# Kernel tuning notes

Hardware: AMD Instinct MI355X
Metric: run time of the kernel (lower is better)

## Reference

```python
import jax, jax.numpy as jnp
import numpy as np

HID = 256
N_HEADS = 4
ATTN_DIM = HID // N_HEADS  # 64
B, S = 64, 512
NEG = -1e10


def setup_inputs() -> dict:
    key = jax.random.key(0)
    ks = jax.random.split(key, 12)
    def lin(k, fan_in, shape):
        bound = 1.0 / np.sqrt(fan_in)
        return jax.random.uniform(k, shape, jnp.float32, -bound, bound)
    return {
        "query": jax.random.normal(ks[0], (B, S, HID), jnp.float32),
        "key": jax.random.normal(ks[1], (B, S, HID), jnp.float32),
        "value": jax.random.normal(ks[2], (B, S, HID), jnp.float32),
        "mask": jax.random.randint(ks[3], (B, 1, S, S), 0, 2, jnp.int32),
        "Wq": lin(ks[4], HID, (HID, HID)), "bq": lin(ks[5], HID, (HID,)),
        "Wk": lin(ks[6], HID, (HID, HID)), "bk": lin(ks[7], HID, (HID,)),
        "Wv": lin(ks[8], HID, (HID, ATTN_DIM)), "bv": lin(ks[9], HID, (ATTN_DIM,)),
        "Wh": lin(ks[10], ATTN_DIM, (ATTN_DIM, HID)), "bh": lin(ks[11], ATTN_DIM, (HID,)),
    }


def reference(query, key, value, mask, Wq, bq, Wk, bk, Wv, bv, Wh, bh):
    b = query.shape[0]
    scale = jnp.sqrt(jnp.asarray(ATTN_DIM, query.dtype))
    Q = (query @ Wq + bq).reshape(b, -1, N_HEADS, ATTN_DIM).transpose(0, 2, 1, 3)  # [B,H,Sq,d]
    K = (key @ Wk + bk).reshape(b, -1, N_HEADS, ATTN_DIM).transpose(0, 2, 1, 3)    # [B,H,Sk,d]
    V = value @ Wv + bv                                                            # [B,Sk,d]
    energy = jnp.einsum('bhqd,bhkd->bhqk', Q, K) / scale
    energy = jnp.where(mask == 0, jnp.asarray(NEG, energy.dtype), energy)
    probs = jax.nn.softmax(energy, axis=-1)          # [B,H,Sq,Sk]
    attention = jnp.mean(probs, axis=1)              # head-mean, [B,Sq,Sk]
    # dropout is identity in eval mode
    output = jnp.einsum('bqk,bkd->bqd', attention, V) @ Wh + bh  # [B,Sq,HID]
    return output, attention
```

## Files before the change

### kernel.cpp

```cpp
#include <hip/hip_runtime.h>

#define NB 64
#define SS 512
#define HIDD 256
#define NHEADS 4
#define ADIM 64
#define NTOT 576

typedef __attribute__((ext_vector_type(8))) short short8v;
typedef __attribute__((ext_vector_type(4))) float f32x4;

#define MFMA16(A, B, C) __builtin_amdgcn_mfma_f32_16x16x32_bf16(A, B, C, 0, 0, 0)
#define AS1 __attribute__((address_space(1)))
#define AS3 __attribute__((address_space(3)))

__device__ __forceinline__ void g2l16(void* lds, const void* g) {
    __builtin_amdgcn_global_load_lds((const AS1 unsigned*)g,
                                     (AS3 unsigned*)lds, 16, 0, 0);
}

__device__ __forceinline__ void bsplit(float x, short& hi, short& lo) {
    unsigned u = __float_as_uint(x);
    unsigned uh = (u + 0x8000u) & 0xFFFF0000u;
    hi = (short)(uh >> 16);
    float r = x - __uint_as_float(uh);
    lo = (short)((__float_as_uint(r) + 0x8000u) >> 16);
}

__device__ __forceinline__ void bsplit_v(float x, short8v& vh, short8v& vl, int i) {
    short h, l;
    bsplit(x, h, l);
    vh[i] = h;
    vl[i] = l;
}

__device__ __forceinline__ short bf16r(float x) {
    return (short)((__float_as_uint(x) + 0x8000u) >> 16);
}

__device__ __forceinline__ int frag_addr(int bb, int hh, int s, int d) {
    const int t16 = s >> 4, rk = s & 15;
    const int ks2 = d >> 5, lgk = (d >> 3) & 3, e8 = d & 7;
    return ((((bb * 4 + hh) * 32 + t16) * 2 + ks2) * 64 + rk + 16 * lgk) * 8 + e8;
}

__global__ __launch_bounds__(256) void prep_weights(
    const float* __restrict__ Wq, const float* __restrict__ Wk,
    const float* __restrict__ Wv, const float* __restrict__ Wh,
    short* __restrict__ WT_hi, short* __restrict__ WT_lo,
    short* __restrict__ WhT)
{
    const int bx = blockIdx.x;
    if (bx < NTOT) {
        const int idx = bx * 256 + threadIdx.x;
        const int n = idx >> 8, k = idx & 255;
        float v;
        if (n < 256)      v = Wq[k * 256 + n];
        else if (n < 512) v = Wk[k * 256 + (n - 256)];
        else              v = Wv[k * 64 + (n - 512)];
        short h, l;
        bsplit(v, h, l);
        WT_hi[idx] = h;
        WT_lo[idx] = l;
    } else {
        const int idx2 = (bx - NTOT) * 256 + threadIdx.x;
        const int n = idx2 >> 6, d = idx2 & 63;
        WhT[idx2] = bf16r(Wh[d * HIDD + n]);
    }
}

__global__ __launch_bounds__(256) void qkv_qk(
    const float* __restrict__ query, const float* __restrict__ key,
    const short* __restrict__ WT_hi, const short* __restrict__ WT_lo,
    const float* __restrict__ bq, const float* __restrict__ bk,
    short* __restrict__ Qhi, short* __restrict__ Khi)
{
    __shared__ short Ws_h[2][128 * 32];
    __shared__ short Ws_l[2][128 * 32];

    const int bm = blockIdx.x * 64;
    const int y = blockIdx.y;
    const int t = y >> 1;
    const int half = y & 1;
    const int nrow0 = t * 256 + half * 128;
    const float* A = t ? key : query;
    const float* biasp = t ? bk : bq;
    short* Dhi = t ? Khi : Qhi;

    const int tid = threadIdx.x;
    const int w = tid >> 6, l = tid & 63;
    const int l15 = l & 15, lg = l >> 4;
    const int wbase = tid & 192;

    auto stageWT = [&](int buf, int kc) {
#pragma unroll
        for (int i = 0; i < 2; ++i) {
            const int g = i * 256 + tid;
            const int row = g >> 2;
            const int p = g & 3;
            const int sl = p ^ (row & 3);
            const size_t goff = (size_t)(nrow0 + row) * HIDD + kc * 32 + sl * 8;
            g2l16(&Ws_h[buf][(i * 256 + wbase) * 8], WT_hi + goff);
            g2l16(&Ws_l[buf][(i * 256 + wbase) * 8], WT_lo + goff);
        }
    };

    const float* arow = A + (size_t)(bm + w * 16 + l15) * HIDD + lg * 8;

    f32x4 acc[8];
#pragma unroll
    for (int jn = 0; jn < 8; ++jn) acc[jn] = (f32x4){0.f, 0.f, 0.f, 0.f};

    float4 a0c = *reinterpret_cast<const float4*>(arow);
    float4 a1c = *reinterpret_cast<const float4*>(arow + 4);
    stageWT(0, 0);
    __syncthreads();

    int cur = 0;
#pragma unroll
    for (int kc = 0; kc < 8; ++kc) {
        float4 a0n, a1n;
        if (kc < 7) {
            a0n = *reinterpret_cast<const float4*>(arow + (kc + 1) * 32);
            a1n = *reinterpret_cast<const float4*>(arow + (kc + 1) * 32 + 4);
            stageWT(cur ^ 1, kc + 1);
        }

        short8v ah, al;
        bsplit_v(a0c.x, ah, al, 0);
        bsplit_v(a0c.y, ah, al, 1);
        bsplit_v(a0c.z, ah, al, 2);
        bsplit_v(a0c.w, ah, al, 3);
        bsplit_v(a1c.x, ah, al, 4);
        bsplit_v(a1c.y, ah, al, 5);
        bsplit_v(a1c.z, ah, al, 6);
        bsplit_v(a1c.w, ah, al, 7);

#pragma unroll
        for (int jn = 0; jn < 8; ++jn) {
            const int rowB = jn * 16 + l15;
            const int c = lg ^ (rowB & 3);
            short8v bh = *reinterpret_cast<const short8v*>(&Ws_h[cur][rowB * 32 + c * 8]);
            short8v bl = *reinterpret_cast<const short8v*>(&Ws_l[cur][rowB * 32 + c * 8]);
            acc[jn] = MFMA16(ah, bh, acc[jn]);
            acc[jn] = MFMA16(ah, bl, acc[jn]);
            acc[jn] = MFMA16(al, bh, acc[jn]);
        }
        __syncthreads();
        cur ^= 1;
        if (kc < 7) { a0c = a0n; a1c = a1n; }
    }

#pragma unroll
    for (int jn = 0; jn < 8; ++jn) {
        const int ncol = half * 128 + jn * 16 + l15;
        const float bias = biasp[ncol];
        const int hh = ncol >> 6, dd = ncol & 63;
#pragma unroll
        for (int r = 0; r < 4; ++r) {
            const int m = bm + w * 16 + lg * 4 + r;
            const int bb = m >> 9, s = m & 511;
            const int fa = frag_addr(bb, hh, s, dd);
            Dhi[fa] = bf16r(acc[jn][r] + bias);
        }
    }
}

__global__ __launch_bounds__(256) void qkv_v(
    const float* __restrict__ value,
    const short* __restrict__ WT_hi, const short* __restrict__ WT_lo,
    const float* __restrict__ bv, short* __restrict__ VT)
{
    __shared__ short Ws_h[2][64 * 32];
    __shared__ short Ws_l[2][64 * 32];

    const int bm = blockIdx.x * 64;
    const int tid = threadIdx.x;
    const int w = tid >> 6, l = tid & 63;
    const int l15 = l & 15, lg = l >> 4;
    const int wbase = tid & 192;

    auto stageWT = [&](int buf, int kc) {
        const int row = tid >> 2;
        const int p = tid & 3;
        const int sl = p ^ (row & 3);
        const size_t goff = (size_t)(512 + row) * HIDD + kc * 32 + sl * 8;
        g2l16(&Ws_h[buf][wbase * 8], WT_hi + goff);
        g2l16(&Ws_l[buf][wbase * 8], WT_lo + goff);
    };

    const float* arow = value + (size_t)(bm + w * 16 + l15) * HIDD + lg * 8;

    f32x4 acc[4];
#pragma unroll
    for (int jn = 0; jn < 4; ++jn) acc[jn] = (f32x4){0.f, 0.f, 0.f, 0.f};

    float4 a0c = *reinterpret_cast<const float4*>(arow);
    float4 a1c = *reinterpret_cast<const float4*>(arow + 4);
    stageWT(0, 0);
    __syncthreads();

    int cur = 0;
#pragma unroll
    for (int kc = 0; kc < 8; ++kc) {
        float4 a0n, a1n;
        if (kc < 7) {
            a0n = *reinterpret_cast<const float4*>(arow + (kc + 1) * 32);
            a1n = *reinterpret_cast<const float4*>(arow + (kc + 1) * 32 + 4);
            stageWT(cur ^ 1, kc + 1);
        }

        short8v ah, al;
        bsplit_v(a0c.x, ah, al, 0);
        bsplit_v(a0c.y, ah, al, 1);
        bsplit_v(a0c.z, ah, al, 2);
        bsplit_v(a0c.w, ah, al, 3);
        bsplit_v(a1c.x, ah, al, 4);
        bsplit_v(a1c.y, ah, al, 5);
        bsplit_v(a1c.z, ah, al, 6);
        bsplit_v(a1c.w, ah, al, 7);

#pragma unroll
        for (int jn = 0; jn < 4; ++jn) {
            const int rowB = jn * 16 + l15;
            const int c = lg ^ (rowB & 3);
            short8v bh = *reinterpret_cast<const short8v*>(&Ws_h[cur][rowB * 32 + c * 8]);
            short8v bl = *reinterpret_cast<const short8v*>(&Ws_l[cur][rowB * 32 + c * 8]);
            acc[jn] = MFMA16(ah, bh, acc[jn]);
            acc[jn] = MFMA16(ah, bl, acc[jn]);
            acc[jn] = MFMA16(al, bh, acc[jn]);
        }
        __syncthreads();
        cur ^= 1;
        if (kc < 7) { a0c = a0n; a1c = a1n; }
    }

#pragma unroll
    for (int jn = 0; jn < 4; ++jn) {
        const int d = jn * 16 + l15;
        const float bias = bv[d];
#pragma unroll
        for (int r = 0; r < 4; ++r) {
            const int m = bm + w * 16 + lg * 4 + r;
            const int bb = m >> 9, kk = m & 511;
            const int ks = kk >> 5;
            const int lane = l15 + 16 * ((kk >> 3) & 3);
            const int idx = (((bb * 4 + jn) * 16 + ks) * 64 + lane) * 8 + (kk & 7);
            VT[idx] = bf16r(acc[jn][r] + bias);
        }
    }
}

__global__ __launch_bounds__(512) void attn_probs_fused(
    const short* __restrict__ Qhi_g, const short* __restrict__ Khi_g,
    const short* __restrict__ VT, const short* __restrict__ WhT,
    const int* __restrict__ mask, const float* __restrict__ bh,
    float* __restrict__ attn, float* __restrict__ out)
{
    __shared__ __align__(16) short P_s[32 * 512];
    __shared__ float red[2][8][2][16];

    const int wg = blockIdx.x;
    const int swz = (wg & 7) * 128 + (wg >> 3);
    const int b = swz >> 4;
    const int q0 = (swz & 15) * 32;

    const int tid = threadIdx.x;
    const int w = tid >> 6;
    const int h2 = w >> 2;
    const int sp = w & 3;
    const int l = tid & 63;
    const int l15 = l & 15;
    const int lg = l >> 4;

    unsigned mbits[2];
#pragma unroll
    for (int qs = 0; qs < 2; ++qs) {
        unsigned bits = 0;
        const int q = q0 + qs * 16 + l15;
        const int* mrow = mask + ((size_t)b * SS + q) * SS;
#pragma unroll
        for (int kl = 0; kl < 2; ++kl)
#pragma unroll
            for (int ms = 0; ms < 2; ++ms) {
                const int fi = kl * 2 + ms;
                const int kt = 2 * h2 + kl;
                const int k = kt * 128 + (2 * sp + ms) * 16 + lg * 4;
                int4 mv = *reinterpret_cast<const int4*>(&mrow[k]);
                bits |= (mv.x != 0 ? 1u : 0u) << (fi * 4 + 0);
                bits |= (mv.y != 0 ? 1u : 0u) << (fi * 4 + 1);
                bits |= (mv.z != 0 ? 1u : 0u) << (fi * 4 + 2);
                bits |= (mv.w != 0 ? 1u : 0u) << (fi * 4 + 3);
            }
        mbits[qs] = bits;
    }

    f32x4 acc[2][2][2];
#pragma unroll
    for (int kl = 0; kl < 2; ++kl)
#pragma unroll
        for (int ms = 0; ms < 2; ++ms)
#pragma unroll
            for (int qs = 0; qs < 2; ++qs)
                acc[kl][ms][qs] = (f32x4){0.f, 0.f, 0.f, 0.f};

    const int qt_base = (swz & 15) * 2;

    for (int h = 0; h < NHEADS; ++h) {
        const int bh32 = (b * 4 + h) * 32;

        short8v qh[2][2];
#pragma unroll
        for (int ks2 = 0; ks2 < 2; ++ks2)
#pragma unroll
            for (int qs = 0; qs < 2; ++qs) {
                const int off = (((bh32 + qt_base + qs) * 2 + ks2) * 64 + l) * 8;
                qh[ks2][qs] = *reinterpret_cast<const short8v*>(Qhi_g + off);
            }

        f32x4 e[2][2][2];
#pragma unroll
        for (int kl = 0; kl < 2; ++kl)
#pragma unroll
            for (int ms = 0; ms < 2; ++ms)
#pragma unroll
                for (int qs = 0; qs < 2; ++qs)
                    e[kl][ms][qs] = (f32x4){0.f, 0.f, 0.f, 0.f};

#pragma unroll
        for (int kl = 0; kl < 2; ++kl) {
            const int t0 = (2 * h2 + kl) * 8 + 2 * sp;
#pragma unroll
            for (int ks2 = 0; ks2 < 2; ++ks2) {
                const int base0 = (((bh32 + t0) * 2 + ks2) * 64 + l) * 8;
                const int base1 = base0 + 1024;
                short8v ah0 = *reinterpret_cast<const short8v*>(Khi_g + base0);
                short8v ah1 = *reinterpret_cast<const short8v*>(Khi_g + base1);

                e[kl][0][0] = MFMA16(ah0, qh[ks2][0], e[kl][0][0]);
                e[kl][0][1] = MFMA16(ah0, qh[ks2][1], e[kl][0][1]);
                e[kl][1][0] = MFMA16(ah1, qh[ks2][0], e[kl][1][0]);
                e[kl][1][1] = MFMA16(ah1, qh[ks2][1], e[kl][1][1]);
            }
        }

        float sm[2] = {0.f, 0.f};
        const float c = 0.125f;
#pragma unroll
        for (int kl = 0; kl < 2; ++kl)
#pragma unroll
            for (int ms = 0; ms < 2; ++ms)
#pragma unroll
                for (int qs = 0; qs < 2; ++qs)
#pragma unroll
                    for (int r = 0; r < 4; ++r) {
                        float p = __expf(e[kl][ms][qs][r] * c);
                        const unsigned bit = (mbits[qs] >> ((kl * 2 + ms) * 4 + r)) & 1u;
                        p = bit ? p : 0.f;
                        e[kl][ms][qs][r] = p;
                        sm[qs] += p;
                    }
#pragma unroll
        for (int qs = 0; qs < 2; ++qs) {
            sm[qs] += __shfl_xor(sm[qs], 16);
            sm[qs] += __shfl_xor(sm[qs], 32);
        }
        if (l < 16) { red[h & 1][w][0][l] = sm[0]; red[h & 1][w][1][l] = sm[1]; }
        __syncthreads();
#pragma unroll
        for (int qs = 0; qs < 2; ++qs) {
            float Z = 0.f;
#pragma unroll
            for (int wv = 0; wv < 8; ++wv) Z += red[h & 1][wv][qs][l15];
            const float inv = 0.25f / fmaxf(Z, 1e-30f);
#pragma unroll
            for (int kl = 0; kl < 2; ++kl)
#pragma unroll
                for (int ms = 0; ms < 2; ++ms)
#pragma unroll
                    for (int r = 0; r < 4; ++r)
                        acc[kl][ms][qs][r] += e[kl][ms][qs][r] * inv;
        }
    }

#pragma unroll
    for (int kl = 0; kl < 2; ++kl)
#pragma unroll
        for (int ms = 0; ms < 2; ++ms)
#pragma unroll
            for (int qs = 0; qs < 2; ++qs) {
                const int kt = 2 * h2 + kl;
                const int q = q0 + qs * 16 + l15;
                const int k = kt * 128 + (2 * sp + ms) * 16 + lg * 4;
                float4 o;
                o.x = acc[kl][ms][qs][0];
                o.y = acc[kl][ms][qs][1];
                o.z = acc[kl][ms][qs][2];
                o.w = acc[kl][ms][qs][3];
                *reinterpret_cast<float4*>(&attn[((size_t)b * SS + q) * SS + k]) = o;

                const int ql_ = qs * 16 + l15;
                const int c8 = kt * 16 + (2 * sp + ms) * 2 + (lg >> 1);
                const int phys = c8 ^ (ql_ & 7);
                short4 pk;
                pk.x = bf16r(acc[kl][ms][qs][0]);
                pk.y = bf16r(acc[kl][ms][qs][1]);
                pk.z = bf16r(acc[kl][ms][qs][2]);
                pk.w = bf16r(acc[kl][ms][qs][3]);
                *reinterpret_cast<short4*>(&P_s[ql_ * 512 + phys * 8 + (lg & 1) * 4]) = pk;
            }
    __syncthreads();

    f32x4 tacc[2];
    tacc[0] = (f32x4){0.f, 0.f, 0.f, 0.f};
    tacc[1] = (f32x4){0.f, 0.f, 0.f, 0.f};
    if (w < 4) {
#pragma unroll
        for (int ks = 0; ks < 16; ++ks) {
            short8v va = *reinterpret_cast<const short8v*>(
                VT + (((b * 4 + w) * 16 + ks) * 64 + l) * 8);
#pragma unroll
            for (int qt = 0; qt < 2; ++qt) {
                const int q = qt * 16 + l15;
                const int phys = (ks * 4 + lg) ^ (q & 7);
                short8v pb = *reinterpret_cast<const short8v*>(&P_s[q * 512 + phys * 8]);
                tacc[qt] = MFMA16(va, pb, tacc[qt]);
            }
        }
    }
    __syncthreads();

    float* T_s = reinterpret_cast<float*>(P_s);
    if (w < 4) {
#pragma unroll
        for (int qt = 0; qt < 2; ++qt) {
            const int q = qt * 16 + l15;
            const int d = w * 16 + lg * 4;
            float4 tv;
            tv.x = tacc[qt][0];
            tv.y = tacc[qt][1];
            tv.z = tacc[qt][2];
            tv.w = tacc[qt][3];
            *reinterpret_cast<float4*>(&T_s[q * 68 + d]) = tv;
        }
    }
    __syncthreads();

    if (w < 4) {
        f32x4 oacc[2][4];
#pragma unroll
        for (int qt = 0; qt < 2; ++qt)
#pragma unroll
            for (int nt = 0; nt < 4; ++nt)
                oacc[qt][nt] = (f32x4){0.f, 0.f, 0.f, 0.f};

#pragma unroll
        for (int ks = 0; ks < 2; ++ks) {
            short8v ta[2];
#pragma unroll
            for (int qt = 0; qt < 2; ++qt) {
                const int q = qt * 16 + l15;
                float4 t0 = *reinterpret_cast<const float4*>(&T_s[q * 68 + ks * 32 + lg * 8]);
                float4 t1 = *reinterpret_cast<const float4*>(&T_s[q * 68 + ks * 32 + lg * 8 + 4]);
                ta[qt][0] = bf16r(t0.x);
                ta[qt][1] = bf16r(t0.y);
                ta[qt][2] = bf16r(t0.z);
                ta[qt][3] = bf16r(t0.w);
                ta[qt][4] = bf16r(t1.x);
                ta[qt][5] = bf16r(t1.y);
                ta[qt][6] = bf16r(t1.z);
                ta[qt][7] = bf16r(t1.w);
            }
#pragma unroll
            for (int nt = 0; nt < 4; ++nt) {
                const int n = (w * 4 + nt) * 16 + l15;
                short8v wb = *reinterpret_cast<const short8v*>(
                    WhT + n * 64 + ks * 32 + lg * 8);
#pragma unroll
                for (int qt = 0; qt < 2; ++qt)
                    oacc[qt][nt] = MFMA16(ta[qt], wb, oacc[qt][nt]);
            }
        }

#pragma unroll
        for (int qt = 0; qt < 2; ++qt)
#pragma unroll
            for (int nt = 0; nt < 4; ++nt) {
                const int n = (w * 4 + nt) * 16 + l15;
                const float bias = bh[n];
#pragma unroll
                for (int r = 0; r < 4; ++r) {
                    const int q = q0 + qt * 16 + lg * 4 + r;
                    out[((size_t)b * SS + q) * HIDD + n] = oacc[qt][nt][r] + bias;
                }
            }
    }
}

extern "C" void kernel_launch(void* const* d_in, const int* in_sizes, int n_in,
                              void* d_out, int out_size, void* d_ws, size_t ws_size,
                              hipStream_t stream)
{
    const float* query = (const float*)d_in[0];
    const float* key   = (const float*)d_in[1];
    const float* value = (const float*)d_in[2];
    const int*   mask  = (const int*)d_in[3];
    const float* Wq = (const float*)d_in[4];
    const float* bq = (const float*)d_in[5];
    const float* Wk = (const float*)d_in[6];
    const float* bk = (const float*)d_in[7];
    const float* Wv = (const float*)d_in[8];
    const float* bv = (const float*)d_in[9];
    const float* Wh = (const float*)d_in[10];
    const float* bh = (const float*)d_in[11];

    float* out  = (float*)d_out;
    float* attn = out + (size_t)NB * SS * HIDD;

    const size_t BS = (size_t)NB * SS;
    short* Qhi = (short*)d_ws;
    short* Khi = Qhi + BS * HIDD;
    short* VT  = Khi + BS * HIDD;
    short* WhT = VT + BS * ADIM;

    short* WT_hi = (short*)attn;
    short* WT_lo = WT_hi + NTOT * HIDD;

    prep_weights<<<dim3(NTOT + 64), 256, 0, stream>>>(Wq, Wk, Wv, Wh,
                                                      WT_hi, WT_lo, WhT);
    qkv_qk<<<dim3(512, 4), 256, 0, stream>>>(query, key, WT_hi, WT_lo,
                                             bq, bk, Qhi, Khi);
    qkv_v<<<dim3(512), 256, 0, stream>>>(value, WT_hi, WT_lo, bv, VT);
    attn_probs_fused<<<dim3(1024), 512, 0, stream>>>(Qhi, Khi, VT, WhT,
                                                     mask, bh, attn, out);
}
```

Before: 137.2 us.

## Shrink attention workgroups to 16 query rows with four waves each

The fused attention kernel now gives each workgroup 16 query rows and 256 threads, launched as 2048 groups instead of 1024 groups of 512 threads covering 32 rows. Each wave handles a contiguous 128-key slice for all four heads, and all four waves now take part in the P·V and output-projection stages, which were previously limited to half the waves. The aim is less idle time in the tail stages, smaller LDS use, and more resident groups. In exchange, each K tile is loaded once per 16 query rows rather than once per 32, which doubles K traffic per query, and the grid swizzle changes.

Measured after the change: 135.3 us. Within noise of the previous version (-1.4%).

```diff
diff --git a/kernel.cpp b/kernel.cpp
--- a/kernel.cpp
+++ b/kernel.cpp
@@ -251,249 +251,185 @@
     }
 }
 
-__global__ __launch_bounds__(512) void attn_probs_fused(
+__global__ __launch_bounds__(256) void attn_probs_fused(
     const short* __restrict__ Qhi_g, const short* __restrict__ Khi_g,
     const short* __restrict__ VT, const short* __restrict__ WhT,
     const int* __restrict__ mask, const float* __restrict__ bh,
     float* __restrict__ attn, float* __restrict__ out)
 {
-    __shared__ __align__(16) short P_s[32 * 512];
-    __shared__ float red[2][8][2][16];
+    __shared__ __align__(16) short P_s[16 * 512];
+    __shared__ float red[2][4][16];
 
     const int wg = blockIdx.x;
-    const int swz = (wg & 7) * 128 + (wg >> 3);
-    const int b = swz >> 4;
-    const int q0 = (swz & 15) * 32;
+    const int swz = (wg & 7) * 256 + (wg >> 3);
+    const int b = swz >> 5;
+    const int qt_base = swz & 31;
+    const int q0 = qt_base * 16;
 
     const int tid = threadIdx.x;
     const int w = tid >> 6;
-    const int h2 = w >> 2;
-    const int sp = w & 3;
     const int l = tid & 63;
     const int l15 = l & 15;
     const int lg = l >> 4;
 
-    unsigned mbits[2];
-#pragma unroll
-    for (int qs = 0; qs < 2; ++qs) {
-        unsigned bits = 0;
-        const int q = q0 + qs * 16 + l15;
+    unsigned mbits = 0;
+    {
+        const int q = q0 + l15;
         const int* mrow = mask + ((size_t)b * SS + q) * SS;
 #pragma unroll
-        for (int kl = 0; kl < 2; ++kl)
-#pragma unroll
-            for (int ms = 0; ms < 2; ++ms) {
-                const int fi = kl * 2 + ms;
-                const int kt = 2 * h2 + kl;
-                const int k = kt * 128 + (2 * sp + ms) * 16 + lg * 4;
-                int4 mv = *reinterpret_cast<const int4*>(&mrow[k]);
-                bits |= (mv.x != 0 ? 1u : 0u) << (fi * 4 + 0);
-                bits |= (mv.y != 0 ? 1u : 0u) << (fi * 4 + 1);
-                bits |= (mv.z != 0 ? 1u : 0u) << (fi * 4 + 2);
-                bits |= (mv.w != 0 ? 1u : 0u) << (fi * 4 + 3);
-            }
-        mbits[qs] = bits;
-    }
-
-    f32x4 acc[2][2][2];
-#pragma unroll
-    for (int kl = 0; kl < 2; ++kl)
-#pragma unroll
-        for (int ms = 0; ms < 2; ++ms)
-#pragma unroll
-            for (int qs = 0; qs < 2; ++qs)
-                acc[kl][ms][qs] = (f32x4){0.f, 0.f, 0.f, 0.f};
-
-    const int qt_base = (swz & 15) * 2;
+        for (int ms = 0; ms < 8; ++ms) {
+            const int k = w * 128 + ms * 16 + lg * 4;
+            int4 mv = *reinterpret_cast<const int4*>(&mrow[k]);
+            mbits |= (mv.x != 0 ? 1u : 0u) << (ms * 4 + 0);
+            mbits |= (mv.y != 0 ? 1u : 0u) << (ms * 4 + 1);
+            mbits |= (mv.z != 0 ? 1u : 0u) << (ms * 4 + 2);
+            mbits |= (mv.w != 0 ? 1u : 0u) << (ms * 4 + 3);
+        }
+    }
+
+    f32x4 acc[8];
+#pragma unroll
+    for (int ms = 0; ms < 8; ++ms) acc[ms] = (f32x4){0.f, 0.f, 0.f, 0.f};
 
     for (int h = 0; h < NHEADS; ++h) {
         const int bh32 = (b * 4 + h) * 32;
 
-        short8v qh[2][2];
-#pragma unroll
-        for (int ks2 = 0; ks2 < 2; ++ks2)
-#pragma unroll
-            for (int qs = 0; qs < 2; ++qs) {
-                const int off = (((bh32 + qt_base + qs) * 2 + ks2) * 64 + l) * 8;
-                qh[ks2][qs] = *reinterpret_cast<const short8v*>(Qhi_g + off);
+        short8v qh[2];
+#pragma unroll
+        for (int ks2 = 0; ks2 < 2; ++ks2) {
+            const int off = (((bh32 + qt_base) * 2 + ks2) * 64 + l) * 8;
+            qh[ks2] = *reinterpret_cast<const short8v*>(Qhi_g + off);
+        }
+
+        f32x4 e[8];
+#pragma unroll
+        for (int ms = 0; ms < 8; ++ms) e[ms] = (f32x4){0.f, 0.f, 0.f, 0.f};
+
+#pragma unroll
+        for (int ms = 0; ms < 8; ++ms) {
+            const int t16 = w * 8 + ms;
+#pragma unroll
+            for (int ks2 = 0; ks2 < 2; ++ks2) {
+                const int base = (((bh32 + t16) * 2 + ks2) * 64 + l) * 8;
+                short8v ah = *reinterpret_cast<const short8v*>(Khi_g + base);
+                e[ms] = MFMA16(ah, qh[ks2], e[ms]);
             }
-
-        f32x4 e[2][2][2];
-#pragma unroll
-        for (int kl = 0; kl < 2; ++kl)
-#pragma unroll
-            for (int ms = 0; ms < 2; ++ms)
-#pragma unroll
-                for (int qs = 0; qs < 2; ++qs)
-                    e[kl][ms][qs] = (f32x4){0.f, 0.f, 0.f, 0.f};
-
-#pragma unroll
-        for (int kl = 0; kl < 2; ++kl) {
-            const int t0 = (2 * h2 + kl) * 8 + 2 * sp;
-#pragma unroll
-            for (int ks2 = 0; ks2 < 2; ++ks2) {
-                const int base0 = (((bh32 + t0) * 2 + ks2) * 64 + l) * 8;
-                const int base1 = base0 + 1024;
-                short8v ah0 = *reinterpret_cast<const short8v*>(Khi_g + base0);
-                short8v ah1 = *reinterpret_cast<const short8v*>(Khi_g + base1);
-
-                e[kl][0][0] = MFMA16(ah0, qh[ks2][0], e[kl][0][0]);
-                e[kl][0][1] = MFMA16(ah0, qh[ks2][1], e[kl][0][1]);
-                e[kl][1][0] = MFMA16(ah1, qh[ks2][0], e[kl][1][0]);
-                e[kl][1][1] = MFMA16(ah1, qh[ks2][1], e[kl][1][1]);
+        }
+
+        float sm = 0.f;
+        const float c = 0.125f;
+#pragma unroll
+        for (int ms = 0; ms < 8; ++ms)
+#pragma unroll
+            for (int r = 0; r < 4; ++r) {
+                float p = __expf(e[ms][r] * c);
+                const unsigned bit = (mbits >> (ms * 4 + r)) & 1u;
+                p = bit ? p : 0.f;
+                e[ms][r] = p;
+                sm += p;
             }
-        }
-
-        float sm[2] = {0.f, 0.f};
-        const float c = 0.125f;
-#pragma unroll
-        for (int kl = 0; kl < 2; ++kl)
-#pragma unroll
-            for (int ms = 0; ms < 2; ++ms)
-#pragma unroll
-                for (int qs = 0; qs < 2; ++qs)
-#pragma unroll
-                    for (int r = 0; r < 4; ++r) {
-                        float p = __expf(e[kl][ms][qs][r] * c);
-                        const unsigned bit = (mbits[qs] >> ((kl * 2 + ms) * 4 + r)) & 1u;
-                        p = bit ? p : 0.f;
-                        e[kl][ms][qs][r] = p;
-                        sm[qs] += p;
-                    }
-#pragma unroll
-        for (int qs = 0; qs < 2; ++qs) {
-            sm[qs] += __shfl_xor(sm[qs], 16);
-            sm[qs] += __shfl_xor(sm[qs], 32);
-        }
-        if (l < 16) { red[h & 1][w][0][l] = sm[0]; red[h & 1][w][1][l] = sm[1]; }
+        sm += __shfl_xor(sm, 16);
+        sm += __shfl_xor(sm, 32);
+        if (l < 16) red[h & 1][w][l] = sm;
         __syncthreads();
-#pragma unroll
-        for (int qs = 0; qs < 2; ++qs) {
-            float Z = 0.f;
-#pragma unroll
-            for (int wv = 0; wv < 8; ++wv) Z += red[h & 1][wv][qs][l15];
+        {
+            const float Z = (red[h & 1][0][l15] + red[h & 1][1][l15]) +
+                            (red[h & 1][2][l15] + red[h & 1][3][l15]);
             const float inv = 0.25f / fmaxf(Z, 1e-30f);
 #pragma unroll
-            for (int kl = 0; kl < 2; ++kl)
-#pragma unroll
-                for (int ms = 0; ms < 2; ++ms)
-#pragma unroll
-                    for (int r = 0; r < 4; ++r)
-                        acc[kl][ms][qs][r] += e[kl][ms][qs][r] * inv;
-        }
-    }
-
-#pragma unroll
-    for (int kl = 0; kl < 2; ++kl)
-#pragma unroll
-        for (int ms = 0; ms < 2; ++ms)
-#pragma unroll
-            for (int qs = 0; qs < 2; ++qs) {
-                const int kt = 2 * h2 + kl;
-                const int q = q0 + qs * 16 + l15;
-                const int k = kt * 128 + (2 * sp + ms) * 16 + lg * 4;
-                float4 o;
-                o.x = acc[kl][ms][qs][0];
-                o.y = acc[kl][ms][qs][1];
-                o.z = acc[kl][ms][qs][2];
-                o.w = acc[kl][ms][qs][3];
-                *reinterpret_cast<float4*>(&attn[((size_t)b * SS + q) * SS + k]) = o;
-
-                const int ql_ = qs * 16 + l15;
-                const int c8 = kt * 16 + (2 * sp + ms) * 2 + (lg >> 1);
-                const int phys = c8 ^ (ql_ & 7);
-                short4 pk;
-                pk.x = bf16r(acc[kl][ms][qs][0]);
-                pk.y = bf16r(acc[kl][ms][qs][1]);
-                pk.z = bf16r(acc[kl][ms][qs][2]);
-                pk.w = bf16r(acc[kl][ms][qs][3]);
-                *reinterpret_cast<short4*>(&P_s[ql_ * 512 + phys * 8 + (lg & 1) * 4]) = pk;
-            }
+            for (int ms = 0; ms < 8; ++ms)
+#pragma unroll
+                for (int r = 0; r < 4; ++r)
+                    acc[ms][r] += e[ms][r] * inv;
+        }
+    }
+
+#pragma unroll
+    for (int ms = 0; ms < 8; ++ms) {
+        const int q = q0 + l15;
+        const int k = w * 128 + ms * 16 + lg * 4;
+        float4 o;
+        o.x = acc[ms][0];
+        o.y = acc[ms][1];
+        o.z = acc[ms][2];
+        o.w = acc[ms][3];
+        *reinterpret_cast<float4*>(&attn[((size_t)b * SS + q) * SS + k]) = o;
+
+        const int ql_ = l15;
+        const int c8 = w * 16 + ms * 2 + (lg >> 1);
+        const int phys = c8 ^ (ql_ & 7);
+        short4 pk;
+        pk.x = bf16r(acc[ms][0]);
+        pk.y = bf16r(acc[ms][1]);
+        pk.z = bf16r(acc[ms][2]);
+        pk.w = bf16r(acc[ms][3]);
+        *reinterpret_cast<short4*>(&P_s[ql_ * 512 + phys * 8 + (lg & 1) * 4]) = pk;
+    }
     __syncthreads();
 
-    f32x4 tacc[2];
-    tacc[0] = (f32x4){0.f, 0.f, 0.f, 0.f};
-    tacc[1] = (f32x4){0.f, 0.f, 0.f, 0.f};
-    if (w < 4) {
-#pragma unroll
-        for (int ks = 0; ks < 16; ++ks) {
-            short8v va = *reinterpret_cast<const short8v*>(
-                VT + (((b * 4 + w) * 16 + ks) * 64 + l) * 8);
-#pragma unroll
-            for (int qt = 0; qt < 2; ++qt) {
-                const int q = qt * 16 + l15;
-                const int phys = (ks * 4 + lg) ^ (q & 7);
-                short8v pb = *reinterpret_cast<const short8v*>(&P_s[q * 512 + phys * 8]);
-                tacc[qt] = MFMA16(va, pb, tacc[qt]);
-            }
-        }
+    f32x4 tacc = (f32x4){0.f, 0.f, 0.f, 0.f};
+#pragma unroll
+    for (int ks = 0; ks < 16; ++ks) {
+        short8v va = *reinterpret_cast<const short8v*>(
+            VT + (((b * 4 + w) * 16 + ks) * 64 + l) * 8);
+        const int q = l15;
+        const int phys = (ks * 4 + lg) ^ (q & 7);
+        short8v pb = *reinterpret_cast<const short8v*>(&P_s[q * 512 + phys * 8]);
+        tacc = MFMA16(va, pb, tacc);
     }
     __syncthreads();
 
     float* T_s = reinterpret_cast<float*>(P_s);
-    if (w < 4) {
-#pragma unroll
-        for (int qt = 0; qt < 2; ++qt) {
-            const int q = qt * 16 + l15;
-            const int d = w * 16 + lg * 4;
-            float4 tv;
-            tv.x = tacc[qt][0];
-            tv.y = tacc[qt][1];
-            tv.z = tacc[qt][2];
-            tv.w = tacc[qt][3];
-            *reinterpret_cast<float4*>(&T_s[q * 68 + d]) = tv;
-        }
+    {
+        const int q = l15;
+        const int d = w * 16 + lg * 4;
+        float4 tv;
+        tv.x = tacc[0];
+        tv.y = tacc[1];
+        tv.z = tacc[2];
+        tv.w = tacc[3];
+        *reinterpret_cast<float4*>(&T_s[q * 68 + d]) = tv;
     }
     __syncthreads();
 
-    if (w < 4) {
-        f32x4 oacc[2][4];
-#pragma unroll
-        for (int qt = 0; qt < 2; ++qt)
-#pragma unroll
-            for (int nt = 0; nt < 4; ++nt)
-                oacc[qt][nt] = (f32x4){0.f, 0.f, 0.f, 0.f};
-
-#pragma unroll
-        for (int ks = 0; ks < 2; ++ks) {
-            short8v ta[2];
-#pragma unroll
-            for (int qt = 0; qt < 2; ++qt) {
-                const int q = qt * 16 + l15;
-                float4 t0 = *reinterpret_cast<const float4*>(&T_s[q * 68 + ks * 32 + lg * 8]);
-                float4 t1 = *reinterpret_cast<const float4*>(&T_s[q * 68 + ks * 32 + lg * 8 + 4]);
-                ta[qt][0] = bf16r(t0.x);
-                ta[qt][1] = bf16r(t0.y);
-                ta[qt][2] = bf16r(t0.z);
-                ta[qt][3] = bf16r(t0.w);
-                ta[qt][4] = bf16r(t1.x);
-                ta[qt][5] = bf16r(t1.y);
-                ta[qt][6] = bf16r(t1.z);
-                ta[qt][7] = bf16r(t1.w);
-            }
-#pragma unroll
-            for (int nt = 0; nt < 4; ++nt) {
-                const int n = (w * 4 + nt) * 16 + l15;
-                short8v wb = *reinterpret_cast<const short8v*>(
-                    WhT + n * 64 + ks * 32 + lg * 8);
-#pragma unroll
-                for (int qt = 0; qt < 2; ++qt)
-                    oacc[qt][nt] = MFMA16(ta[qt], wb, oacc[qt][nt]);
-            }
-        }
-
-#pragma unroll
-        for (int qt = 0; qt < 2; ++qt)
-#pragma unroll
-            for (int nt = 0; nt < 4; ++nt) {
-                const int n = (w * 4 + nt) * 16 + l15;
-                const float bias = bh[n];
-#pragma unroll
-                for (int r = 0; r < 4; ++r) {
-                    const int q = q0 + qt * 16 + lg * 4 + r;
-                    out[((size_t)b * SS + q) * HIDD + n] = oacc[qt][nt][r] + bias;
-                }
-            }
+    f32x4 oacc[4];
+#pragma unroll
+    for (int nt = 0; nt < 4; ++nt) oacc[nt] = (f32x4){0.f, 0.f, 0.f, 0.f};
+
+#pragma unroll
+    for (int ks = 0; ks < 2; ++ks) {
+        short8v ta;
+        {
+            const int q = l15;
+            float4 t0 = *reinterpret_cast<const float4*>(&T_s[q * 68 + ks * 32 + lg * 8]);
+            float4 t1 = *reinterpret_cast<const float4*>(&T_s[q * 68 + ks * 32 + lg * 8 + 4]);
+            ta[0] = bf16r(t0.x);
+            ta[1] = bf16r(t0.y);
+            ta[2] = bf16r(t0.z);
+            ta[3] = bf16r(t0.w);
+            ta[4] = bf16r(t1.x);
+            ta[5] = bf16r(t1.y);
+            ta[6] = bf16r(t1.z);
+            ta[7] = bf16r(t1.w);
+        }
+#pragma unroll
+        for (int nt = 0; nt < 4; ++nt) {
+            const int n = (w * 4 + nt) * 16 + l15;
+            short8v wb = *reinterpret_cast<const short8v*>(
+                WhT + n * 64 + ks * 32 + lg * 8);
+            oacc[nt] = MFMA16(ta, wb, oacc[nt]);
+        }
+    }
+
+#pragma unroll
+    for (int nt = 0; nt < 4; ++nt) {
+        const int n = (w * 4 + nt) * 16 + l15;
+        const float bias = bh[n];
+#pragma unroll
+        for (int r = 0; r < 4; ++r) {
+            const int q = q0 + lg * 4 + r;
+            out[((size_t)b * SS + q) * HIDD + n] = oacc[nt][r] + bias;
+        }
     }
 }
 
@@ -531,6 +467,6 @@
     qkv_qk<<<dim3(512, 4), 256, 0, stream>>>(query, key, WT_hi, WT_lo,
                                              bq, bk, Qhi, Khi);
     qkv_v<<<dim3(512), 256, 0, stream>>>(value, WT_hi, WT_lo, bv, VT);
-    attn_probs_fused<<<dim3(1024), 512, 0, stream>>>(Qhi, Khi, VT, WhT,
+    attn_probs_fused<<<dim3(2048), 256, 0, stream>>>(Qhi, Khi, VT, WhT,
                                                      mask, bh, attn, out);
 }
```
